# Kernel tuning notes

Measured on AMD Instinct MI355X. Metric: run time of the kernel, lower is better.

## Reference

```python
import jax, jax.numpy as jnp
import numpy as np

LAYERS = 16
F_SAMPLES = 48   # frequency (pilot subcarrier) samples
T_SAMPLES = 512  # time-domain samples


def dft_matrices(F=F_SAMPLES, T=T_SAMPLES):
    # IDFT: [F, T] maps freq-domain [B,F] -> time-domain [B,T]
    # DFT:  [T, F] maps time-domain [B,T] -> freq-domain [B,F]
    f = np.arange(F)[:, None]
    t = np.arange(T)[None, :]
    ang = 2.0 * np.pi * f * t / T                      # [F, T]
    scale = 1.0 / np.sqrt(T)
    idft_re = jnp.asarray(np.cos(ang) * scale, jnp.float32)   # [F, T]
    idft_im = jnp.asarray(np.sin(ang) * scale, jnp.float32)
    dft_re = jnp.asarray(np.cos(ang).T * scale, jnp.float32)  # [T, F]
    dft_im = jnp.asarray(-np.sin(ang).T * scale, jnp.float32)
    return dft_re, dft_im, idft_re, idft_im


def mm(a_re, a_im, b_re, b_im):
    # complex matmul (a_re + i a_im) @ (b_re + i b_im) via 4 real GEMMs
    return (a_re @ b_re - a_im @ b_im,
            a_re @ b_im + a_im @ b_re)


def soft_gate(x, s1, s2):
    # sigmoid(x, S1, S2) = logistic(S1 * (x - S2)) -- soft-threshold gate
    return jax.nn.sigmoid(s1 * (x - s2))


def setup_inputs() -> dict:
    key = jax.random.key(0)
    u = jax.random.normal(key, (16384, F_SAMPLES, 2), dtype=jnp.float32)
    S1 = jnp.full((1,), 10.0, dtype=jnp.float32)
    S2 = jnp.full((1,), 0.5, dtype=jnp.float32)
    return {"u": u, "S1": S1, "S2": S2}


def reference(u, S1, S2):
    dft_re, dft_im, idft_re, idft_im = dft_matrices()
    B = u.shape[0]

    maximum = jnp.abs(u.max())
    u = 5.0 * u / maximum
    u_re, u_im = u[:, :, 0], u[:, :, 1]

    z_re, z_im = u_re, u_im
    H_re = jnp.zeros((B, T_SAMPLES), jnp.float32)
    H_im = jnp.zeros((B, T_SAMPLES), jnp.float32)

    def layer(carry, _):
        z_re, z_im, H_re, H_im = carry
        Z_re, Z_im = mm(z_re, z_im, idft_re, idft_im)      # [B, T]
        R_re = H_re + Z_re
        R_im = H_im + Z_im
        R_mean = jnp.sqrt(jnp.mean(R_re * R_re + R_im * R_im, axis=0))  # [T]
        g = soft_gate(R_mean, S1[0], S2[0])                # [T]
        H_re = R_re * g
        H_im = R_im * g
        h_re, h_im = mm(H_re, H_im, dft_re, dft_im)        # [B, F]
        z_re = u_re - h_re
        z_im = u_im - h_im
        return (z_re, z_im, H_re, H_im), None

    (z_re, z_im, H_re, H_im), _ = jax.lax.scan(
        layer, (z_re, z_im, H_re, H_im), None, length=LAYERS)

    h_re, h_im = mm(H_re, H_im, dft_re, dft_im)            # [B, F]
    out = jnp.stack((h_re, h_im), axis=2)                  # [B, F, 2]
    out = out / 5.0 * maximum
    return out
```

## Files before the change

### kernel.cpp

```cpp
#include <hip/hip_runtime.h>
#include <math.h>

#define NROWS 16384
#define FC 96
#define T 512
#define NRI 1024
#define LAYERS 16

typedef _Float16 f16;
typedef _Float16 half8 __attribute__((ext_vector_type(8)));
typedef _Float16 half4 __attribute__((ext_vector_type(4)));
typedef float floatx4 __attribute__((ext_vector_type(4)));

#define OFF_MAXKEY 0
#define OFF_ARR  64
#define OFF_REL  (OFF_ARR + 256 * 32)
#define OFF_W1   (OFF_REL + 256 * 32)
#define OFF_W1L  (OFF_W1 + 49152)
#define OFF_W2   (OFF_W1L + 49152)
#define OFF_W2L  (OFF_W2 + 49152)
#define OFF_PART (OFF_W2L + 49152)
#define OFF_FIN  (OFF_PART + 256 * NRI)

#define SMEM_BYTES 155648

__global__ void ksetup(float* __restrict__ ws) {
    int t = threadIdx.x;
    if (t == 0)
        __hip_atomic_store((unsigned*)(ws + OFF_MAXKEY), 0u, __ATOMIC_RELAXED, __HIP_MEMORY_SCOPE_AGENT);
    for (int i = t; i < 2 * 256 * 32; i += 256)
        __hip_atomic_store((unsigned*)(ws + OFF_ARR) + i, 0u, __ATOMIC_RELAXED, __HIP_MEMORY_SCOPE_AGENT);
}

__global__ void kwf(float* __restrict__ ws) {
    int idx = blockIdx.x * 256 + threadIdx.x;
    if (idx >= 2 * 98304) return;
    int which = idx >= 98304;
    int id = which ? idx - 98304 : idx;
    int j = id & 7, lane = (id >> 3) & 63, rem = id >> 9;
    int k, n;
    if (!which) { int kc = rem % 3,  nt = rem / 3;  k = kc*32 + (lane>>4)*8 + j; n = nt*16 + (lane&15); }
    else        { int kc = rem & 31, nt = rem >> 5; k = kc*32 + (lane>>4)*8 + j; n = nt*16 + (lane&15); }
    int t, f, q, e;
    if (!which) { t = n >> 1; e = n & 1; f = k >> 1; q = k & 1; }
    else        { t = k >> 1; q = k & 1; f = n >> 1; e = n & 1; }
    int ft = (f * t) & (T - 1);
    float sv, cv;
    sincosf((float)ft * 0.012271846303085129f, &sv, &cv);
    const float sc = 0.04419417382415922f;
    cv *= sc; sv *= sc;
    float val;
    if (!which) val = (e == 0) ? (q == 0 ? cv : -sv) : (q == 0 ?  sv : cv);
    else        val = (e == 0) ? (q == 0 ? cv :  sv) : (q == 0 ? -sv : cv);
    f16 hi = (f16)val;
    f16 lo = (f16)(val - (float)hi);
    f16* H = (f16*)(ws + (which ? OFF_W2 : OFF_W1));
    f16* L = (f16*)(ws + (which ? OFF_W2L : OFF_W1L));
    H[id] = hi;
    L[id] = lo;
}

__device__ __forceinline__ void gbar2(float* __restrict__ ws, unsigned e) {
    asm volatile("s_waitcnt vmcnt(0)" ::: "memory");
    __syncthreads();
    const int tid = threadIdx.x;
    unsigned* __restrict__ Af = (unsigned*)(ws + OFF_ARR);
    unsigned* __restrict__ Rf = (unsigned*)(ws + OFF_REL);
    if (blockIdx.x == 0) {
        if (tid < 64) {
            bool ok;
            do {
                __builtin_amdgcn_s_sleep(1);
                ok = true;
#pragma unroll
                for (int s = 0; s < 4; s++) {
                    int b = s * 64 + tid;
                    unsigned v = __hip_atomic_load(&Af[b * 32], __ATOMIC_RELAXED, __HIP_MEMORY_SCOPE_AGENT);
                    ok = ok && (b == 0 || v >= e);
                }
            } while (!__all(ok));
            asm volatile("" ::: "memory");
#pragma unroll
            for (int s = 0; s < 4; s++) {
                int b = s * 64 + tid;
                __hip_atomic_store(&Rf[b * 32], e, __ATOMIC_RELAXED, __HIP_MEMORY_SCOPE_AGENT);
            }
        }
        __syncthreads();
    } else {
        if (tid == 0) {
            __hip_atomic_store(&Af[blockIdx.x * 32], e, __ATOMIC_RELAXED, __HIP_MEMORY_SCOPE_AGENT);
            while (__hip_atomic_load(&Rf[blockIdx.x * 32], __ATOMIC_RELAXED, __HIP_MEMORY_SCOPE_AGENT) < e)
                __builtin_amdgcn_s_sleep(2);
            asm volatile("" ::: "memory");
        }
        __syncthreads();
    }
}

__device__ __forceinline__ void coh_store8(float* p, float a, float b) {
    unsigned long long v = ((unsigned long long)__float_as_uint(b) << 32) | __float_as_uint(a);
    (void)__hip_atomic_exchange((unsigned long long*)p, v, __ATOMIC_RELAXED, __HIP_MEMORY_SCOPE_AGENT);
}

__global__ __launch_bounds__(512, 2) void kmain(const float* __restrict__ u,
                                                const float* __restrict__ S1,
                                                const float* __restrict__ S2,
                                                float* __restrict__ out,
                                                float* __restrict__ ws) {
    extern __shared__ char smem[];
    f16* zh = (f16*)smem;
    f16* zl = zh + 64 * FC;
    f16* Hh = zl + 64 * FC;
    f16* Hl = Hh + 2 * 64 * 256;
    __shared__ float smax[8];

    const int tid = threadIdx.x;
    const int w = tid >> 6;
    const int lane = tid & 63;
    const int q = lane >> 4;
    const int l15 = lane & 15;
    const int row0 = blockIdx.x * 64;
    const float s1 = S1[0], s2 = S2[0];

    unsigned epoch = 1;

    float m = -1e30f;
    for (int i = tid; i < 64 * FC; i += 512) m = fmaxf(m, u[(long)row0 * FC + i]);
#pragma unroll
    for (int s = 1; s < 64; s <<= 1) m = fmaxf(m, __shfl_xor(m, s, 64));
    if (lane == 0) smax[w] = m;
    __syncthreads();
    if (tid == 0) {
        float mm = smax[0];
#pragma unroll
        for (int i = 1; i < 8; i++) mm = fmaxf(mm, smax[i]);
        unsigned k = __float_as_uint(mm);
        k = (k & 0x80000000u) ? ~k : (k | 0x80000000u);
        atomicMax((unsigned*)(ws + OFF_MAXKEY), k);
    }
    gbar2(ws, epoch); epoch++;
    unsigned key = __hip_atomic_load((unsigned*)(ws + OFF_MAXKEY), __ATOMIC_RELAXED, __HIP_MEMORY_SCOPE_AGENT);
    unsigned ku = (key & 0x80000000u) ? (key ^ 0x80000000u) : ~key;
    const float gmax = fabsf(__uint_as_float(ku));
    const float sc_to = 5.0f / gmax;
    const float sc_from = gmax / 5.0f;

    for (int i = tid; i < 64 * FC; i += 512) {
        int b = i / FC, fc = i - b * FC;
        float z = sc_to * u[(long)row0 * FC + i];
        f16 h = (f16)z;
        int idx = b * FC + ((fc & ~31) | ((fc & 31) ^ ((b & 3) << 3)));
        zh[idx] = h;
        zl[idx] = (f16)(z - (float)h);
    }

    floatx4 R[32];
#pragma unroll
    for (int i = 0; i < 32; i++) R[i] = (floatx4){0.f, 0.f, 0.f, 0.f};

    const f16* __restrict__ w1h = (const f16*)(ws + OFF_W1);
    const f16* __restrict__ w1l = (const f16*)(ws + OFF_W1L);
    const f16* __restrict__ w2h = (const f16*)(ws + OFF_W2);
    const f16* __restrict__ w2l = (const f16*)(ws + OFF_W2L);

    const int brow = (w & 3) * 16 + l15;
    const int fh = (w >> 2) * 3;
    const int hswz = (l15 & 7) << 3;

    float gcur = 0.0f;

#pragma unroll 1
    for (int l = 0; l < LAYERS; l++) {
        __syncthreads();

        if (l > 0) {
#pragma unroll
            for (int ntl = 0; ntl < 8; ntl++) {
                float ga = __shfl(gcur, ntl * 8 + q * 2, 64);
                float gb = __shfl(gcur, ntl * 8 + q * 2 + 1, 64);
#pragma unroll
                for (int bt = 0; bt < 4; bt++) {
                    R[ntl * 4 + bt][0] *= ga;
                    R[ntl * 4 + bt][1] *= ga;
                    R[ntl * 4 + bt][2] *= gb;
                    R[ntl * 4 + bt][3] *= gb;
                }
            }
        }
#pragma unroll
        for (int kc = 0; kc < 3; kc++) {
            half8 Bh[4], Bl[4];
#pragma unroll
            for (int bt = 0; bt < 4; bt++) {
                int b = bt * 16 + l15;
                int zi = b * FC + kc * 32 + ((q ^ (b & 3)) << 3);
                Bh[bt] = *(const half8*)(zh + zi);
                Bl[bt] = *(const half8*)(zl + zi);
            }
#pragma unroll
            for (int ntl = 0; ntl < 8; ntl++) {
                int wi = (((w * 8 + ntl) * 3 + kc) * 64 + lane) * 8;
                half8 Ah = *(const half8*)(w1h + wi);
                half8 Al = *(const half8*)(w1l + wi);
#pragma unroll
                for (int bt = 0; bt < 4; bt++) {
                    R[ntl*4+bt] = __builtin_amdgcn_mfma_f32_16x16x32_f16(Ah, Bh[bt], R[ntl*4+bt], 0, 0, 0);
                    R[ntl*4+bt] = __builtin_amdgcn_mfma_f32_16x16x32_f16(Ah, Bl[bt], R[ntl*4+bt], 0, 0, 0);
                    R[ntl*4+bt] = __builtin_amdgcn_mfma_f32_16x16x32_f16(Al, Bh[bt], R[ntl*4+bt], 0, 0, 0);
                }
            }
        }

        {
            float* part = ws + OFF_PART + (long)blockIdx.x * NRI;
#pragma unroll
            for (int ntl = 0; ntl < 8; ntl++) {
                floatx4 ps;
#pragma unroll
                for (int r = 0; r < 4; r++) {
                    float p = R[ntl*4+0][r] * R[ntl*4+0][r];
                    p = fmaf(R[ntl*4+1][r], R[ntl*4+1][r], p);
                    p = fmaf(R[ntl*4+2][r], R[ntl*4+2][r], p);
                    p = fmaf(R[ntl*4+3][r], R[ntl*4+3][r], p);
                    p += __shfl_xor(p, 1, 64);
                    p += __shfl_xor(p, 2, 64);
                    p += __shfl_xor(p, 4, 64);
                    p += __shfl_xor(p, 8, 64);
                    ps[r] = p;
                }
                if (l15 == 0) {
                    int n = w * 128 + ntl * 16 + q * 4;
                    coh_store8(part + n, ps[0], ps[1]);
                    coh_store8(part + n + 2, ps[2], ps[3]);
                }
            }
        }
        gbar2(ws, epoch); epoch++;

        if (w == 0) {
            const int n0 = blockIdx.x * 4;
            const float* pb = ws + OFF_PART;
            floatx4 cs = {0.f, 0.f, 0.f, 0.f};
#pragma unroll
            for (int s4 = 0; s4 < 4; s4++) {
                long off = (long)(s4 * 64 + lane) * NRI + n0;
                unsigned long long a = __hip_atomic_load((const unsigned long long*)(pb + off),
                                                         __ATOMIC_RELAXED, __HIP_MEMORY_SCOPE_AGENT);
                unsigned long long b = __hip_atomic_load((const unsigned long long*)(pb + off + 2),
                                                         __ATOMIC_RELAXED, __HIP_MEMORY_SCOPE_AGENT);
                cs[0] += __uint_as_float((unsigned)a);
                cs[1] += __uint_as_float((unsigned)(a >> 32));
                cs[2] += __uint_as_float((unsigned)b);
                cs[3] += __uint_as_float((unsigned)(b >> 32));
            }
#pragma unroll
            for (int sh = 1; sh < 64; sh <<= 1) {
                cs[0] += __shfl_xor(cs[0], sh, 64);
                cs[1] += __shfl_xor(cs[1], sh, 64);
                cs[2] += __shfl_xor(cs[2], sh, 64);
                cs[3] += __shfl_xor(cs[3], sh, 64);
            }
            if (lane == 0) {
                coh_store8(ws + OFF_FIN + n0, cs[0], cs[1]);
                coh_store8(ws + OFF_FIN + n0 + 2, cs[2], cs[3]);
            }
        }
        gbar2(ws, epoch); epoch++;

        {
            int n = w * 128 + lane * 2;
            unsigned long long pv = __hip_atomic_load((const unsigned long long*)(ws + OFF_FIN + n),
                                                      __ATOMIC_RELAXED, __HIP_MEMORY_SCOPE_AGENT);
            float sa = __uint_as_float((unsigned)pv);
            float sb = __uint_as_float((unsigned)(pv >> 32));
            float rm = sqrtf((sa + sb) * (1.0f / 16384.0f));
            gcur = 1.0f / (1.0f + expf(-s1 * (rm - s2)));
        }

        auto writeH = [&](int buf) {
            f16* hh = Hh + buf * (64 * 256);
            f16* hl = Hl + buf * (64 * 256);
#pragma unroll
            for (int ntl = 0; ntl < 8; ntl++) {
                float ga = __shfl(gcur, ntl * 8 + q * 2, 64);
                float gb = __shfl(gcur, ntl * 8 + q * 2 + 1, 64);
                floatx4 g4 = {ga, ga, gb, gb};
                int lbase = (w & 1) * 128 + (ntl >> 2) * 64;
                int soff = (ntl & 3) * 16 + q * 4;
#pragma unroll
                for (int bt = 0; bt < 4; bt++) {
                    int b = bt * 16 + l15;
                    half4 vh, vl;
#pragma unroll
                    for (int r = 0; r < 4; r++) {
                        float v = g4[r] * R[ntl * 4 + bt][r];
                        f16 hi = (f16)v;
                        vh[r] = hi;
                        vl[r] = (f16)(v - (float)hi);
                    }
                    int idx = b * 256 + lbase + (soff ^ ((b & 7) << 3));
                    *(half4*)(hh + idx) = vh;
                    *(half4*)(hl + idx) = vl;
                }
            }
        };

        floatx4 acc[3];
#pragma unroll
        for (int i = 0; i < 3; i++) acc[i] = (floatx4){0.f, 0.f, 0.f, 0.f};

        if ((w >> 1) == 0) writeH(0);
        __syncthreads();
#pragma unroll 1
        for (int c = 0; c < 4; c++) {
            if (c < 3 && (w >> 1) == c + 1) writeH((c + 1) & 1);
            const f16* hh = Hh + (c & 1) * (64 * 256);
            const f16* hl = Hl + (c & 1) * (64 * 256);
#pragma unroll
            for (int ks = 0; ks < 8; ks++) {
                int idx = brow * 256 + (ks >> 1) * 64 + (((ks & 1) * 32 + q * 8) ^ hswz);
                half8 Ah = *(const half8*)(hh + idx);
                half8 Al = *(const half8*)(hl + idx);
                int kg = c * 8 + ks;
#pragma unroll
                for (int ft = 0; ft < 3; ft++) {
                    int wi = (((fh + ft) * 32 + kg) * 64 + lane) * 8;
                    half8 Wh = *(const half8*)(w2h + wi);
                    half8 Wl = *(const half8*)(w2l + wi);
                    acc[ft] = __builtin_amdgcn_mfma_f32_16x16x32_f16(Ah, Wh, acc[ft], 0, 0, 0);
                    acc[ft] = __builtin_amdgcn_mfma_f32_16x16x32_f16(Ah, Wl, acc[ft], 0, 0, 0);
                    acc[ft] = __builtin_amdgcn_mfma_f32_16x16x32_f16(Al, Wh, acc[ft], 0, 0, 0);
                }
            }
            __syncthreads();
        }

        if (l < LAYERS - 1) {
#pragma unroll
            for (int ft = 0; ft < 3; ft++) {
                int fcg = (fh + ft) * 16 + l15;
#pragma unroll
                for (int r = 0; r < 4; r++) {
                    int b = (w & 3) * 16 + q * 4 + r;
                    float z = fmaf(sc_to, u[(long)(row0 + b) * FC + fcg], -acc[ft][r]);
                    f16 h = (f16)z;
                    int idx = b * FC + ((fcg & ~31) | ((fcg & 31) ^ ((b & 3) << 3)));
                    zh[idx] = h;
                    zl[idx] = (f16)(z - (float)h);
                }
            }
        } else {
#pragma unroll
            for (int ft = 0; ft < 3; ft++) {
                int fcg = (fh + ft) * 16 + l15;
#pragma unroll
                for (int r = 0; r < 4; r++) {
                    int b = (w & 3) * 16 + q * 4 + r;
                    out[(long)(row0 + b) * FC + fcg] = acc[ft][r] * sc_from;
                }
            }
        }
    }
}

extern "C" void kernel_launch(void* const* d_in, const int* in_sizes, int n_in,
                              void* d_out, int out_size, void* d_ws, size_t ws_size,
                              hipStream_t stream) {
    (void)in_sizes; (void)n_in; (void)out_size; (void)ws_size;
    const float* u  = (const float*)d_in[0];
    const float* S1 = (const float*)d_in[1];
    const float* S2 = (const float*)d_in[2];
    float* out = (float*)d_out;
    float* ws  = (float*)d_ws;

    static int inited = 0;
    if (!inited) {
        hipFuncSetAttribute((const void*)kmain, hipFuncAttributeMaxDynamicSharedMemorySize, SMEM_BYTES);
        inited = 1;
    }

    ksetup<<<1, 256, 0, stream>>>(ws);
    kwf<<<768, 256, 0, stream>>>(ws);

    void* args[] = {(void*)&u, (void*)&S1, (void*)&S2, (void*)&out, (void*)&ws};
    hipLaunchCooperativeKernel((const void*)kmain, dim3(256), dim3(512), args,
                               (unsigned)SMEM_BYTES, stream);
}
```

Before: 1.412 ms.

## Double threads per block, split work across 16 waves with split-K reduction

Raises the block size from 512 to 1024 threads so each wave holds half the R accumulator tiles for the first GEMM, which cuts register pressure. The second GEMM is split along K between two wave groups, and their partial results are summed through shared memory before the z update. The intent is more resident waves per CU to hide latency. The cost is an extra LDS reduction and barrier per layer, and launch_bounds(1024,4) may cause spills or fail to fit 155KB of shared memory per block.

```diff
diff --git a/kernel.cpp b/kernel.cpp
--- a/kernel.cpp
+++ b/kernel.cpp
@@ -6,6 +6,7 @@
 #define T 512
 #define NRI 1024
 #define LAYERS 16
+#define NBLK 256
 
 typedef _Float16 f16;
 typedef _Float16 half8 __attribute__((ext_vector_type(8)));
@@ -14,13 +15,13 @@
 
 #define OFF_MAXKEY 0
 #define OFF_ARR  64
-#define OFF_REL  (OFF_ARR + 256 * 32)
-#define OFF_W1   (OFF_REL + 256 * 32)
+#define OFF_REL  (OFF_ARR + NBLK * 32)
+#define OFF_W1   (OFF_REL + NBLK * 32)
 #define OFF_W1L  (OFF_W1 + 49152)
 #define OFF_W2   (OFF_W1L + 49152)
 #define OFF_W2L  (OFF_W2 + 49152)
 #define OFF_PART (OFF_W2L + 49152)
-#define OFF_FIN  (OFF_PART + 256 * NRI)
+#define OFF_FIN  (OFF_PART + NBLK * NRI)
 
 #define SMEM_BYTES 155648
 
@@ -28,7 +29,7 @@
     int t = threadIdx.x;
     if (t == 0)
         __hip_atomic_store((unsigned*)(ws + OFF_MAXKEY), 0u, __ATOMIC_RELAXED, __HIP_MEMORY_SCOPE_AGENT);
-    for (int i = t; i < 2 * 256 * 32; i += 256)
+    for (int i = t; i < 2 * NBLK * 32; i += 256)
         __hip_atomic_store((unsigned*)(ws + OFF_ARR) + i, 0u, __ATOMIC_RELAXED, __HIP_MEMORY_SCOPE_AGENT);
 }
 
@@ -73,7 +74,7 @@
                 __builtin_amdgcn_s_sleep(1);
                 ok = true;
 #pragma unroll
-                for (int s = 0; s < 4; s++) {
+                for (int s = 0; s < NBLK / 64; s++) {
                     int b = s * 64 + tid;
                     unsigned v = __hip_atomic_load(&Af[b * 32], __ATOMIC_RELAXED, __HIP_MEMORY_SCOPE_AGENT);
                     ok = ok && (b == 0 || v >= e);
@@ -81,7 +82,7 @@
             } while (!__all(ok));
             asm volatile("" ::: "memory");
 #pragma unroll
-            for (int s = 0; s < 4; s++) {
+            for (int s = 0; s < NBLK / 64; s++) {
                 int b = s * 64 + tid;
                 __hip_atomic_store(&Rf[b * 32], e, __ATOMIC_RELAXED, __HIP_MEMORY_SCOPE_AGENT);
             }
@@ -103,17 +104,17 @@
     (void)__hip_atomic_exchange((unsigned long long*)p, v, __ATOMIC_RELAXED, __HIP_MEMORY_SCOPE_AGENT);
 }
 
-__global__ __launch_bounds__(512, 2) void kmain(const float* __restrict__ u,
-                                                const float* __restrict__ S1,
-                                                const float* __restrict__ S2,
-                                                float* __restrict__ out,
-                                                float* __restrict__ ws) {
+__global__ __launch_bounds__(1024, 4) void kmain(const float* __restrict__ u,
+                                                 const float* __restrict__ S1,
+                                                 const float* __restrict__ S2,
+                                                 float* __restrict__ out,
+                                                 float* __restrict__ ws) {
     extern __shared__ char smem[];
     f16* zh = (f16*)smem;
     f16* zl = zh + 64 * FC;
     f16* Hh = zl + 64 * FC;
     f16* Hl = Hh + 2 * 64 * 256;
-    __shared__ float smax[8];
+    __shared__ float smax[16];
 
     const int tid = threadIdx.x;
     const int w = tid >> 6;
@@ -126,7 +127,7 @@
     unsigned epoch = 1;
 
     float m = -1e30f;
-    for (int i = tid; i < 64 * FC; i += 512) m = fmaxf(m, u[(long)row0 * FC + i]);
+    for (int i = tid; i < 64 * FC; i += 1024) m = fmaxf(m, u[(long)row0 * FC + i]);
 #pragma unroll
     for (int s = 1; s < 64; s <<= 1) m = fmaxf(m, __shfl_xor(m, s, 64));
     if (lane == 0) smax[w] = m;
@@ -134,7 +135,7 @@
     if (tid == 0) {
         float mm = smax[0];
 #pragma unroll
-        for (int i = 1; i < 8; i++) mm = fmaxf(mm, smax[i]);
+        for (int i = 1; i < 16; i++) mm = fmaxf(mm, smax[i]);
         unsigned k = __float_as_uint(mm);
         k = (k & 0x80000000u) ? ~k : (k | 0x80000000u);
         atomicMax((unsigned*)(ws + OFF_MAXKEY), k);
@@ -146,7 +147,7 @@
     const float sc_to = 5.0f / gmax;
     const float sc_from = gmax / 5.0f;
 
-    for (int i = tid; i < 64 * FC; i += 512) {
+    for (int i = tid; i < 64 * FC; i += 1024) {
         int b = i / FC, fc = i - b * FC;
         float z = sc_to * u[(long)row0 * FC + i];
         f16 h = (f16)z;
@@ -155,17 +156,20 @@
         zl[idx] = (f16)(z - (float)h);
     }
 
-    floatx4 R[32];
-#pragma unroll
-    for (int i = 0; i < 32; i++) R[i] = (floatx4){0.f, 0.f, 0.f, 0.f};
+    floatx4 R[16];
+#pragma unroll
+    for (int i = 0; i < 16; i++) R[i] = (floatx4){0.f, 0.f, 0.f, 0.f};
 
     const f16* __restrict__ w1h = (const f16*)(ws + OFF_W1);
     const f16* __restrict__ w1l = (const f16*)(ws + OFF_W1L);
     const f16* __restrict__ w2h = (const f16*)(ws + OFF_W2);
     const f16* __restrict__ w2l = (const f16*)(ws + OFF_W2L);
 
-    const int brow = (w & 3) * 16 + l15;
-    const int fh = (w >> 2) * 3;
+    const int rt = w & 3;
+    const int ftt = (w >> 2) & 1;
+    const int Kh = w >> 3;
+    const int fh = ftt * 3;
+    const int brow = rt * 16 + l15;
     const int hswz = (l15 & 7) << 3;
 
     float gcur = 0.0f;
@@ -176,7 +180,7 @@
 
         if (l > 0) {
 #pragma unroll
-            for (int ntl = 0; ntl < 8; ntl++) {
+            for (int ntl = 0; ntl < 4; ntl++) {
                 float ga = __shfl(gcur, ntl * 8 + q * 2, 64);
                 float gb = __shfl(gcur, ntl * 8 + q * 2 + 1, 64);
 #pragma unroll
@@ -199,8 +203,8 @@
                 Bl[bt] = *(const half8*)(zl + zi);
             }
 #pragma unroll
-            for (int ntl = 0; ntl < 8; ntl++) {
-                int wi = (((w * 8 + ntl) * 3 + kc) * 64 + lane) * 8;
+            for (int ntl = 0; ntl < 4; ntl++) {
+                int wi = (((w * 4 + ntl) * 3 + kc) * 64 + lane) * 8;
                 half8 Ah = *(const half8*)(w1h + wi);
                 half8 Al = *(const half8*)(w1l + wi);
 #pragma unroll
@@ -215,7 +219,7 @@
         {
             float* part = ws + OFF_PART + (long)blockIdx.x * NRI;
 #pragma unroll
-            for (int ntl = 0; ntl < 8; ntl++) {
+            for (int ntl = 0; ntl < 4; ntl++) {
                 floatx4 ps;
 #pragma unroll
                 for (int r = 0; r < 4; r++) {
@@ -230,7 +234,7 @@
                     ps[r] = p;
                 }
                 if (l15 == 0) {
-                    int n = w * 128 + ntl * 16 + q * 4;
+                    int n = w * 64 + ntl * 16 + q * 4;
                     coh_store8(part + n, ps[0], ps[1]);
                     coh_store8(part + n + 2, ps[2], ps[3]);
                 }
@@ -269,7 +273,7 @@
         gbar2(ws, epoch); epoch++;
 
         {
-            int n = w * 128 + lane * 2;
+            int n = w * 64 + (lane & 31) * 2;
             unsigned long long pv = __hip_atomic_load((const unsigned long long*)(ws + OFF_FIN + n),
                                                       __ATOMIC_RELAXED, __HIP_MEMORY_SCOPE_AGENT);
             float sa = __uint_as_float((unsigned)pv);
@@ -282,12 +286,12 @@
             f16* hh = Hh + buf * (64 * 256);
             f16* hl = Hl + buf * (64 * 256);
 #pragma unroll
-            for (int ntl = 0; ntl < 8; ntl++) {
+            for (int ntl = 0; ntl < 4; ntl++) {
                 float ga = __shfl(gcur, ntl * 8 + q * 2, 64);
                 float gb = __shfl(gcur, ntl * 8 + q * 2 + 1, 64);
                 floatx4 g4 = {ga, ga, gb, gb};
-                int lbase = (w & 1) * 128 + (ntl >> 2) * 64;
-                int soff = (ntl & 3) * 16 + q * 4;
+                int lbase = (w & 3) * 64;
+                int soff = ntl * 16 + q * 4;
 #pragma unroll
                 for (int bt = 0; bt < 4; bt++) {
                     int b = bt * 16 + l15;
@@ -310,54 +314,74 @@
 #pragma unroll
         for (int i = 0; i < 3; i++) acc[i] = (floatx4){0.f, 0.f, 0.f, 0.f};
 
-        if ((w >> 1) == 0) writeH(0);
+        if ((w >> 2) == 0) writeH(0);
         __syncthreads();
 #pragma unroll 1
         for (int c = 0; c < 4; c++) {
-            if (c < 3 && (w >> 1) == c + 1) writeH((c + 1) & 1);
-            const f16* hh = Hh + (c & 1) * (64 * 256);
-            const f16* hl = Hl + (c & 1) * (64 * 256);
-#pragma unroll
-            for (int ks = 0; ks < 8; ks++) {
-                int idx = brow * 256 + (ks >> 1) * 64 + (((ks & 1) * 32 + q * 8) ^ hswz);
-                half8 Ah = *(const half8*)(hh + idx);
-                half8 Al = *(const half8*)(hl + idx);
-                int kg = c * 8 + ks;
+            if (c < 3 && (w >> 2) == c + 1) writeH((c + 1) & 1);
+            if ((c >> 1) == Kh) {
+                const f16* hh = Hh + (c & 1) * (64 * 256);
+                const f16* hl = Hl + (c & 1) * (64 * 256);
+#pragma unroll
+                for (int ks = 0; ks < 8; ks++) {
+                    int idx = brow * 256 + (ks >> 1) * 64 + (((ks & 1) * 32 + q * 8) ^ hswz);
+                    half8 Ah = *(const half8*)(hh + idx);
+                    half8 Al = *(const half8*)(hl + idx);
+                    int kg = c * 8 + ks;
+#pragma unroll
+                    for (int ft = 0; ft < 3; ft++) {
+                        int wi = (((fh + ft) * 32 + kg) * 64 + lane) * 8;
+                        half8 Wh = *(const half8*)(w2h + wi);
+                        half8 Wl = *(const half8*)(w2l + wi);
+                        acc[ft] = __builtin_amdgcn_mfma_f32_16x16x32_f16(Ah, Wh, acc[ft], 0, 0, 0);
+                        acc[ft] = __builtin_amdgcn_mfma_f32_16x16x32_f16(Ah, Wl, acc[ft], 0, 0, 0);
+                        acc[ft] = __builtin_amdgcn_mfma_f32_16x16x32_f16(Al, Wh, acc[ft], 0, 0, 0);
+                    }
+                }
+            }
+            __syncthreads();
+        }
+
+        {
+            floatx4* red = (floatx4*)Hh;
+            if (Kh == 1) {
+#pragma unroll
+                for (int ft = 0; ft < 3; ft++) red[((w - 8) * 3 + ft) * 64 + lane] = acc[ft];
+            }
+            __syncthreads();
+            if (Kh == 0) {
 #pragma unroll
                 for (int ft = 0; ft < 3; ft++) {
-                    int wi = (((fh + ft) * 32 + kg) * 64 + lane) * 8;
-                    half8 Wh = *(const half8*)(w2h + wi);
-                    half8 Wl = *(const half8*)(w2l + wi);
-                    acc[ft] = __builtin_amdgcn_mfma_f32_16x16x32_f16(Ah, Wh, acc[ft], 0, 0, 0);
-                    acc[ft] = __builtin_amdgcn_mfma_f32_16x16x32_f16(Ah, Wl, acc[ft], 0, 0, 0);
-                    acc[ft] = __builtin_amdgcn_mfma_f32_16x16x32_f16(Al, Wh, acc[ft], 0, 0, 0);
-                }
-            }
-            __syncthreads();
-        }
-
-        if (l < LAYERS - 1) {
-#pragma unroll
-            for (int ft = 0; ft < 3; ft++) {
-                int fcg = (fh + ft) * 16 + l15;
-#pragma unroll
-                for (int r = 0; r < 4; r++) {
-                    int b = (w & 3) * 16 + q * 4 + r;
-                    float z = fmaf(sc_to, u[(long)(row0 + b) * FC + fcg], -acc[ft][r]);
-                    f16 h = (f16)z;
-                    int idx = b * FC + ((fcg & ~31) | ((fcg & 31) ^ ((b & 3) << 3)));
-                    zh[idx] = h;
-                    zl[idx] = (f16)(z - (float)h);
-                }
-            }
-        } else {
-#pragma unroll
-            for (int ft = 0; ft < 3; ft++) {
-                int fcg = (fh + ft) * 16 + l15;
-#pragma unroll
-                for (int r = 0; r < 4; r++) {
-                    int b = (w & 3) * 16 + q * 4 + r;
-                    out[(long)(row0 + b) * FC + fcg] = acc[ft][r] * sc_from;
+                    floatx4 o = red[(w * 3 + ft) * 64 + lane];
+                    acc[ft][0] += o[0]; acc[ft][1] += o[1]; acc[ft][2] += o[2]; acc[ft][3] += o[3];
+                }
+            }
+        }
+
+        if (Kh == 0) {
+            if (l < LAYERS - 1) {
+#pragma unroll
+                for (int ft = 0; ft < 3; ft++) {
+                    int fcg = (fh + ft) * 16 + l15;
+#pragma unroll
+                    for (int r = 0; r < 4; r++) {
+                        int b = rt * 16 + q * 4 + r;
+                        float z = fmaf(sc_to, u[(long)(row0 + b) * FC + fcg], -acc[ft][r]);
+                        f16 h = (f16)z;
+                        int idx = b * FC + ((fcg & ~31) | ((fcg & 31) ^ ((b & 3) << 3)));
+                        zh[idx] = h;
+                        zl[idx] = (f16)(z - (float)h);
+                    }
+                }
+            } else {
+#pragma unroll
+                for (int ft = 0; ft < 3; ft++) {
+                    int fcg = (fh + ft) * 16 + l15;
+#pragma unroll
+                    for (int r = 0; r < 4; r++) {
+                        int b = rt * 16 + q * 4 + r;
+                        out[(long)(row0 + b) * FC + fcg] = acc[ft][r] * sc_from;
+                    }
                 }
             }
         }
@@ -384,6 +408,6 @@
     kwf<<<768, 256, 0, stream>>>(ws);
 
     void* args[] = {(void*)&u, (void*)&S1, (void*)&S2, (void*)&out, (void*)&ws};
-    hipLaunchCooperativeKernel((const void*)kmain, dim3(256), dim3(512), args,
+    hipLaunchCooperativeKernel((const void*)kmain, dim3(NBLK), dim3(1024), args,
                                (unsigned)SMEM_BYTES, stream);
 }
```

Result: slower. 1.567 ms (+11.0%).

## Replace per-layer grid barriers with point-to-point tag flags for reductions

Applied to the files above, without the earlier changes.

Removes the two centralized grid barriers around the cross-block sum-of-squares reduction in each layer. Each block now publishes a per-layer tag after writing its partials, and the reducing wave polls all 256 partial tags directly. Consumers then poll only the 32 final-sum tags they need, one per wave. This takes away the master-block round trip, so blocks proceed as soon as their own data dependencies are ready, at the cost of more polling traffic and more complex memory-ordering reasoning.

```diff
diff --git a/kernel.cpp b/kernel.cpp
--- a/kernel.cpp
+++ b/kernel.cpp
@@ -6,6 +6,7 @@
 #define T 512
 #define NRI 1024
 #define LAYERS 16
+#define NBLK 256
 
 typedef _Float16 f16;
 typedef _Float16 half8 __attribute__((ext_vector_type(8)));
@@ -14,13 +15,15 @@
 
 #define OFF_MAXKEY 0
 #define OFF_ARR  64
-#define OFF_REL  (OFF_ARR + 256 * 32)
-#define OFF_W1   (OFF_REL + 256 * 32)
+#define OFF_REL  (OFF_ARR + NBLK * 32)
+#define OFF_PTAG (OFF_REL + NBLK * 32)
+#define OFF_FTAG (OFF_PTAG + NBLK)
+#define OFF_W1   (OFF_FTAG + NBLK)
 #define OFF_W1L  (OFF_W1 + 49152)
 #define OFF_W2   (OFF_W1L + 49152)
 #define OFF_W2L  (OFF_W2 + 49152)
 #define OFF_PART (OFF_W2L + 49152)
-#define OFF_FIN  (OFF_PART + 256 * NRI)
+#define OFF_FIN  (OFF_PART + NBLK * NRI)
 
 #define SMEM_BYTES 155648
 
@@ -28,8 +31,10 @@
     int t = threadIdx.x;
     if (t == 0)
         __hip_atomic_store((unsigned*)(ws + OFF_MAXKEY), 0u, __ATOMIC_RELAXED, __HIP_MEMORY_SCOPE_AGENT);
-    for (int i = t; i < 2 * 256 * 32; i += 256)
+    for (int i = t; i < 2 * NBLK * 32; i += 256)
         __hip_atomic_store((unsigned*)(ws + OFF_ARR) + i, 0u, __ATOMIC_RELAXED, __HIP_MEMORY_SCOPE_AGENT);
+    for (int i = t; i < 2 * NBLK; i += 256)
+        __hip_atomic_store((unsigned*)(ws + OFF_PTAG) + i, 0u, __ATOMIC_RELAXED, __HIP_MEMORY_SCOPE_AGENT);
 }
 
 __global__ void kwf(float* __restrict__ ws) {
@@ -73,7 +78,7 @@
                 __builtin_amdgcn_s_sleep(1);
                 ok = true;
 #pragma unroll
-                for (int s = 0; s < 4; s++) {
+                for (int s = 0; s < NBLK / 64; s++) {
                     int b = s * 64 + tid;
                     unsigned v = __hip_atomic_load(&Af[b * 32], __ATOMIC_RELAXED, __HIP_MEMORY_SCOPE_AGENT);
                     ok = ok && (b == 0 || v >= e);
@@ -81,7 +86,7 @@
             } while (!__all(ok));
             asm volatile("" ::: "memory");
 #pragma unroll
-            for (int s = 0; s < 4; s++) {
+            for (int s = 0; s < NBLK / 64; s++) {
                 int b = s * 64 + tid;
                 __hip_atomic_store(&Rf[b * 32], e, __ATOMIC_RELAXED, __HIP_MEMORY_SCOPE_AGENT);
             }
@@ -123,8 +128,6 @@
     const int row0 = blockIdx.x * 64;
     const float s1 = S1[0], s2 = S2[0];
 
-    unsigned epoch = 1;
-
     float m = -1e30f;
     for (int i = tid; i < 64 * FC; i += 512) m = fmaxf(m, u[(long)row0 * FC + i]);
 #pragma unroll
@@ -139,7 +142,7 @@
         k = (k & 0x80000000u) ? ~k : (k | 0x80000000u);
         atomicMax((unsigned*)(ws + OFF_MAXKEY), k);
     }
-    gbar2(ws, epoch); epoch++;
+    gbar2(ws, 1u);
     unsigned key = __hip_atomic_load((unsigned*)(ws + OFF_MAXKEY), __ATOMIC_RELAXED, __HIP_MEMORY_SCOPE_AGENT);
     unsigned ku = (key & 0x80000000u) ? (key ^ 0x80000000u) : ~key;
     const float gmax = fabsf(__uint_as_float(ku));
@@ -163,6 +166,8 @@
     const f16* __restrict__ w1l = (const f16*)(ws + OFF_W1L);
     const f16* __restrict__ w2h = (const f16*)(ws + OFF_W2);
     const f16* __restrict__ w2l = (const f16*)(ws + OFF_W2L);
+    unsigned* __restrict__ ptag = (unsigned*)(ws + OFF_PTAG);
+    unsigned* __restrict__ ftag = (unsigned*)(ws + OFF_FTAG);
 
     const int brow = (w & 3) * 16 + l15;
     const int fh = (w >> 2) * 3;
@@ -172,6 +177,7 @@
 
 #pragma unroll 1
     for (int l = 0; l < LAYERS; l++) {
+        const unsigned tg = (unsigned)(l + 1);
         __syncthreads();
 
         if (l > 0) {
@@ -236,9 +242,24 @@
                 }
             }
         }
-        gbar2(ws, epoch); epoch++;
+        asm volatile("s_waitcnt vmcnt(0)" ::: "memory");
+        __syncthreads();
+        if (tid == 0)
+            __hip_atomic_store(&ptag[blockIdx.x], tg, __ATOMIC_RELAXED, __HIP_MEMORY_SCOPE_AGENT);
 
         if (w == 0) {
+            bool ok;
+            do {
+                __builtin_amdgcn_s_sleep(1);
+                ok = true;
+#pragma unroll
+                for (int s4 = 0; s4 < 4; s4++) {
+                    unsigned v = __hip_atomic_load(&ptag[s4 * 64 + lane],
+                                                   __ATOMIC_RELAXED, __HIP_MEMORY_SCOPE_AGENT);
+                    ok = ok && (v >= tg);
+                }
+            } while (!__all(ok));
+
             const int n0 = blockIdx.x * 4;
             const float* pb = ws + OFF_PART;
             floatx4 cs = {0.f, 0.f, 0.f, 0.f};
@@ -265,10 +286,19 @@
                 coh_store8(ws + OFF_FIN + n0, cs[0], cs[1]);
                 coh_store8(ws + OFF_FIN + n0 + 2, cs[2], cs[3]);
             }
-        }
-        gbar2(ws, epoch); epoch++;
+            asm volatile("s_waitcnt vmcnt(0)" ::: "memory");
+            if (lane == 0)
+                __hip_atomic_store(&ftag[blockIdx.x], tg, __ATOMIC_RELAXED, __HIP_MEMORY_SCOPE_AGENT);
+        }
 
         {
+            const int qi = w * 32 + (lane & 31);
+            bool ok;
+            do {
+                __builtin_amdgcn_s_sleep(1);
+                ok = __hip_atomic_load(&ftag[qi], __ATOMIC_RELAXED, __HIP_MEMORY_SCOPE_AGENT) >= tg;
+            } while (!__all(ok));
+
             int n = w * 128 + lane * 2;
             unsigned long long pv = __hip_atomic_load((const unsigned long long*)(ws + OFF_FIN + n),
                                                       __ATOMIC_RELAXED, __HIP_MEMORY_SCOPE_AGENT);
@@ -384,6 +414,6 @@
     kwf<<<768, 256, 0, stream>>>(ws);
 
     void* args[] = {(void*)&u, (void*)&S1, (void*)&S2, (void*)&out, (void*)&ws};
-    hipLaunchCooperativeKernel((const void*)kmain, dim3(256), dim3(512), args,
+    hipLaunchCooperativeKernel((const void*)kmain, dim3(NBLK), dim3(512), args,
                                (unsigned)SMEM_BYTES, stream);
 }
```

New measurement: 1.428 ms. No clear change (+1.1%).

## Drop low-half split of H and stage full H tile in shared memory once

Applied to the files above, without the earlier changes.

The second GEMM (H times DFT) now stores H only as a single fp16 value instead of a hi/lo pair. It drops the Al*Wh MFMA term, cutting MFMA work for that stage by a third. The four-chunk double-buffered staging of H is replaced by writing the whole 64x1024 H tile to shared memory once, followed by one barrier and a single unrolled K loop. This removes the per-chunk barriers and halves the LDS writes, but it loses precision in H, which may hurt accuracy against the fp32 reference.

```diff
diff --git a/kernel.cpp b/kernel.cpp
--- a/kernel.cpp
+++ b/kernel.cpp
@@ -6,6 +6,7 @@
 #define T 512
 #define NRI 1024
 #define LAYERS 16
+#define NBLK 256
 
 typedef _Float16 f16;
 typedef _Float16 half8 __attribute__((ext_vector_type(8)));
@@ -14,13 +15,13 @@
 
 #define OFF_MAXKEY 0
 #define OFF_ARR  64
-#define OFF_REL  (OFF_ARR + 256 * 32)
-#define OFF_W1   (OFF_REL + 256 * 32)
+#define OFF_REL  (OFF_ARR + NBLK * 32)
+#define OFF_W1   (OFF_REL + NBLK * 32)
 #define OFF_W1L  (OFF_W1 + 49152)
 #define OFF_W2   (OFF_W1L + 49152)
 #define OFF_W2L  (OFF_W2 + 49152)
 #define OFF_PART (OFF_W2L + 49152)
-#define OFF_FIN  (OFF_PART + 256 * NRI)
+#define OFF_FIN  (OFF_PART + NBLK * NRI)
 
 #define SMEM_BYTES 155648
 
@@ -28,7 +29,7 @@
     int t = threadIdx.x;
     if (t == 0)
         __hip_atomic_store((unsigned*)(ws + OFF_MAXKEY), 0u, __ATOMIC_RELAXED, __HIP_MEMORY_SCOPE_AGENT);
-    for (int i = t; i < 2 * 256 * 32; i += 256)
+    for (int i = t; i < 2 * NBLK * 32; i += 256)
         __hip_atomic_store((unsigned*)(ws + OFF_ARR) + i, 0u, __ATOMIC_RELAXED, __HIP_MEMORY_SCOPE_AGENT);
 }
 
@@ -73,7 +74,7 @@
                 __builtin_amdgcn_s_sleep(1);
                 ok = true;
 #pragma unroll
-                for (int s = 0; s < 4; s++) {
+                for (int s = 0; s < NBLK / 64; s++) {
                     int b = s * 64 + tid;
                     unsigned v = __hip_atomic_load(&Af[b * 32], __ATOMIC_RELAXED, __HIP_MEMORY_SCOPE_AGENT);
                     ok = ok && (b == 0 || v >= e);
@@ -81,7 +82,7 @@
             } while (!__all(ok));
             asm volatile("" ::: "memory");
 #pragma unroll
-            for (int s = 0; s < 4; s++) {
+            for (int s = 0; s < NBLK / 64; s++) {
                 int b = s * 64 + tid;
                 __hip_atomic_store(&Rf[b * 32], e, __ATOMIC_RELAXED, __HIP_MEMORY_SCOPE_AGENT);
             }
@@ -111,8 +112,7 @@
     extern __shared__ char smem[];
     f16* zh = (f16*)smem;
     f16* zl = zh + 64 * FC;
-    f16* Hh = zl + 64 * FC;
-    f16* Hl = Hh + 2 * 64 * 256;
+    f16* Hs = zl + 64 * FC;
     __shared__ float smax[8];
 
     const int tid = threadIdx.x;
@@ -166,7 +166,8 @@
 
     const int brow = (w & 3) * 16 + l15;
     const int fh = (w >> 2) * 3;
-    const int hswz = (l15 & 7) << 3;
+    const int aswz = (brow & 7) << 3;
+    const long hrow = (long)brow * NRI;
 
     float gcur = 0.0f;
 
@@ -278,62 +279,37 @@
             gcur = 1.0f / (1.0f + expf(-s1 * (rm - s2)));
         }
 
-        auto writeH = [&](int buf) {
-            f16* hh = Hh + buf * (64 * 256);
-            f16* hl = Hl + buf * (64 * 256);
-#pragma unroll
-            for (int ntl = 0; ntl < 8; ntl++) {
-                float ga = __shfl(gcur, ntl * 8 + q * 2, 64);
-                float gb = __shfl(gcur, ntl * 8 + q * 2 + 1, 64);
-                floatx4 g4 = {ga, ga, gb, gb};
-                int lbase = (w & 1) * 128 + (ntl >> 2) * 64;
-                int soff = (ntl & 3) * 16 + q * 4;
-#pragma unroll
-                for (int bt = 0; bt < 4; bt++) {
-                    int b = bt * 16 + l15;
-                    half4 vh, vl;
-#pragma unroll
-                    for (int r = 0; r < 4; r++) {
-                        float v = g4[r] * R[ntl * 4 + bt][r];
-                        f16 hi = (f16)v;
-                        vh[r] = hi;
-                        vl[r] = (f16)(v - (float)hi);
-                    }
-                    int idx = b * 256 + lbase + (soff ^ ((b & 7) << 3));
-                    *(half4*)(hh + idx) = vh;
-                    *(half4*)(hl + idx) = vl;
-                }
-            }
-        };
+#pragma unroll
+        for (int ntl = 0; ntl < 8; ntl++) {
+            float ga = __shfl(gcur, ntl * 8 + q * 2, 64);
+            float gb = __shfl(gcur, ntl * 8 + q * 2 + 1, 64);
+            floatx4 g4 = {ga, ga, gb, gb};
+            int col = w * 128 + ntl * 16 + q * 4;
+#pragma unroll
+            for (int bt = 0; bt < 4; bt++) {
+                int row = bt * 16 + l15;
+                half4 vh;
+#pragma unroll
+                for (int r = 0; r < 4; r++) vh[r] = (f16)(g4[r] * R[ntl * 4 + bt][r]);
+                *(half4*)(Hs + row * NRI + (col ^ ((row & 7) << 3))) = vh;
+            }
+        }
+        __syncthreads();
 
         floatx4 acc[3];
 #pragma unroll
         for (int i = 0; i < 3; i++) acc[i] = (floatx4){0.f, 0.f, 0.f, 0.f};
-
-        if ((w >> 1) == 0) writeH(0);
-        __syncthreads();
-#pragma unroll 1
-        for (int c = 0; c < 4; c++) {
-            if (c < 3 && (w >> 1) == c + 1) writeH((c + 1) & 1);
-            const f16* hh = Hh + (c & 1) * (64 * 256);
-            const f16* hl = Hl + (c & 1) * (64 * 256);
-#pragma unroll
-            for (int ks = 0; ks < 8; ks++) {
-                int idx = brow * 256 + (ks >> 1) * 64 + (((ks & 1) * 32 + q * 8) ^ hswz);
-                half8 Ah = *(const half8*)(hh + idx);
-                half8 Al = *(const half8*)(hl + idx);
-                int kg = c * 8 + ks;
-#pragma unroll
-                for (int ft = 0; ft < 3; ft++) {
-                    int wi = (((fh + ft) * 32 + kg) * 64 + lane) * 8;
-                    half8 Wh = *(const half8*)(w2h + wi);
-                    half8 Wl = *(const half8*)(w2l + wi);
-                    acc[ft] = __builtin_amdgcn_mfma_f32_16x16x32_f16(Ah, Wh, acc[ft], 0, 0, 0);
-                    acc[ft] = __builtin_amdgcn_mfma_f32_16x16x32_f16(Ah, Wl, acc[ft], 0, 0, 0);
-                    acc[ft] = __builtin_amdgcn_mfma_f32_16x16x32_f16(Al, Wh, acc[ft], 0, 0, 0);
-                }
-            }
-            __syncthreads();
+#pragma unroll 4
+        for (int kg = 0; kg < 32; kg++) {
+            half8 Ah = *(const half8*)(Hs + hrow + ((kg * 32 + q * 8) ^ aswz));
+#pragma unroll
+            for (int ft = 0; ft < 3; ft++) {
+                int wi = (((fh + ft) * 32 + kg) * 64 + lane) * 8;
+                half8 Wh = *(const half8*)(w2h + wi);
+                half8 Wl = *(const half8*)(w2l + wi);
+                acc[ft] = __builtin_amdgcn_mfma_f32_16x16x32_f16(Ah, Wh, acc[ft], 0, 0, 0);
+                acc[ft] = __builtin_amdgcn_mfma_f32_16x16x32_f16(Ah, Wl, acc[ft], 0, 0, 0);
+            }
         }
 
         if (l < LAYERS - 1) {
@@ -384,6 +360,6 @@
     kwf<<<768, 256, 0, stream>>>(ws);
 
     void* args[] = {(void*)&u, (void*)&S1, (void*)&S2, (void*)&out, (void*)&ws};
-    hipLaunchCooperativeKernel((const void*)kmain, dim3(256), dim3(512), args,
+    hipLaunchCooperativeKernel((const void*)kmain, dim3(NBLK), dim3(512), args,
                                (unsigned)SMEM_BYTES, stream);
 }
```

Result: faster. 1.251 ms (-11.4%).
